# Optimization experiments

Measured on AMD Instinct MI355X. Metric: run time of the kernel, lower is better.

## Reference

```python
import jax, jax.numpy as jnp
import numpy as np

BS = 128          # block size for fp8 block-scaled quantization
FP8_MAX = 448.0   # max normal value of float8_e4m3fn


def _weight_quant(w):
    """Quantize weight [O, I] with per-(128x128)-block scales, DeepSeek-V3 style.
    Returns (w_q stored as fp32 holding fp8-representable values, scale [O/BS, I/BS])."""
    O, I = w.shape
    wb = w.reshape(O // BS, BS, I // BS, BS)
    amax = jnp.max(jnp.abs(wb), axis=(1, 3))
    scale = jnp.where(amax == 0, 1.0, amax / FP8_MAX)
    q = (wb / scale[:, None, :, None]).astype(jnp.float8_e4m3fn).astype(jnp.float32)
    return q.reshape(O, I), scale


def _act_qdq(x):
    """act_quant + dequant: per-128-block (last dim) fp8 quantization of activations."""
    T, D = x.shape
    xb = x.reshape(T, D // BS, BS)
    amax = jnp.max(jnp.abs(xb), axis=-1, keepdims=True)
    scale = jnp.where(amax == 0, 1.0, amax / FP8_MAX)
    q = (xb / scale).astype(jnp.float8_e4m3fn).astype(jnp.float32)
    return (q * scale).reshape(T, D)


def _dequant_w(wq, ws):
    O, I = wq.shape
    return (wq.reshape(O // BS, BS, I // BS, BS) * ws[:, None, :, None]).reshape(O, I)


def _linear_fp8(x, wq, ws):
    # fp8_gemm with per-block scales == dequantized GEMM in fp32 accumulate
    return _act_qdq(x) @ _dequant_w(wq, ws).T


def setup_inputs() -> dict:
    T, DIM, INTER = 2048, 4096, 11008
    key = jax.random.key(0)
    kx, k1, k2, k3 = jax.random.split(key, 4)
    x = jax.random.normal(kx, (T, DIM), dtype=jnp.float32)
    w1 = jax.random.normal(k1, (INTER, DIM), dtype=jnp.float32) * 0.02
    w2 = jax.random.normal(k2, (DIM, INTER), dtype=jnp.float32) * 0.02
    w3 = jax.random.normal(k3, (INTER, DIM), dtype=jnp.float32) * 0.02
    w1_q, w1_s = _weight_quant(w1)
    w2_q, w2_s = _weight_quant(w2)
    w3_q, w3_s = _weight_quant(w3)
    return {"x": x, "w1_q": w1_q, "w1_s": w1_s, "w2_q": w2_q, "w2_s": w2_s,
            "w3_q": w3_q, "w3_s": w3_s}


def reference(x, w1_q, w1_s, w2_q, w2_s, w3_q, w3_s):
    # SwiGLU: w2( silu(w1(x)) * w3(x) ), each linear is fp8 block-scaled GEMM
    h = jax.nn.silu(_linear_fp8(x, w1_q, w1_s)) * _linear_fp8(x, w3_q, w3_s)
    return _linear_fp8(h, w2_q, w2_s)
```

## Files before the change

kernel.cpp:

```cpp
#include <hip/hip_runtime.h>
#include <hip/hip_fp8.h>

#define T_DIM 2048
#define D_DIM 4096
#define I_DIM 11008

typedef int v8i __attribute__((ext_vector_type(8)));
typedef float v4f __attribute__((ext_vector_type(4)));

__device__ inline unsigned char to_fp8(float f) {
  return (unsigned char)__hip_cvt_float_to_fp8(f, __HIP_SATFINITE, __HIP_E4M3);
}

__device__ inline void async_copy16(const void* g, void* l) {
  __builtin_amdgcn_global_load_lds((const __attribute__((address_space(1))) void*)g,
                                   (__attribute__((address_space(3))) void*)l, 16, 0, 0);
}

__global__ void quant_x_kernel(const float* __restrict__ X, unsigned char* __restrict__ Q,
                               float* __restrict__ St, const int T, const int D) {
  const int wave = (blockIdx.x << 2) + (threadIdx.x >> 6);
  const int lane = threadIdx.x & 63;
  const int nb = D >> 7;
  const int t = wave / nb;
  const int kb = wave - t * nb;
  const size_t base = (size_t)t * D + ((size_t)kb << 7);
  const float2 v = ((const float2*)(X + base))[lane];
  float a = fmaxf(fabsf(v.x), fabsf(v.y));
#pragma unroll
  for (int off = 32; off > 0; off >>= 1) a = fmaxf(a, __shfl_xor(a, off));
  const float scale = (a == 0.f) ? 1.f : (a / 448.f);
  unsigned short pk = (unsigned short)to_fp8(v.x / scale) |
                      ((unsigned short)to_fp8(v.y / scale) << 8);
  ((unsigned short*)(Q + base))[lane] = pk;
  if (lane == 0) St[(size_t)kb * T + t] = scale;
}

__global__ void silu_mul_quant_kernel(const float* __restrict__ H1, const float* __restrict__ H3,
                                      unsigned char* __restrict__ Q, float* __restrict__ St,
                                      const int T, const int D) {
  const int wave = (blockIdx.x << 2) + (threadIdx.x >> 6);
  const int lane = threadIdx.x & 63;
  const int nb = D >> 7;
  const int t = wave / nb;
  const int kb = wave - t * nb;
  const size_t base = (size_t)t * D + ((size_t)kb << 7);
  const float2 v1 = ((const float2*)(H1 + base))[lane];
  const float2 v3 = ((const float2*)(H3 + base))[lane];
  const float hx = (v1.x / (1.f + expf(-v1.x))) * v3.x;
  const float hy = (v1.y / (1.f + expf(-v1.y))) * v3.y;
  float a = fmaxf(fabsf(hx), fabsf(hy));
#pragma unroll
  for (int off = 32; off > 0; off >>= 1) a = fmaxf(a, __shfl_xor(a, off));
  const float scale = (a == 0.f) ? 1.f : (a / 448.f);
  unsigned short pk = (unsigned short)to_fp8(hx / scale) |
                      ((unsigned short)to_fp8(hy / scale) << 8);
  ((unsigned short*)(Q + base))[lane] = pk;
  if (lane == 0) St[(size_t)kb * T + t] = scale;
}

__global__ void convert_fp8_kernel(const float4* __restrict__ W, unsigned int* __restrict__ Q,
                                   const int n4) {
  const int i = blockIdx.x * 256 + threadIdx.x;
  if (i >= n4) return;
  const float4 f = W[i];
  Q[i] = (unsigned int)to_fp8(f.x) | ((unsigned int)to_fp8(f.y) << 8) |
         ((unsigned int)to_fp8(f.z) << 16) | ((unsigned int)to_fp8(f.w) << 24);
}

__global__ __launch_bounds__(256, 2) void gemm_fp8_bs(
    const unsigned char* __restrict__ A, const float* __restrict__ sAt,
    const unsigned char* __restrict__ B, const float* __restrict__ sB,
    float* __restrict__ C, const int M, const int N, const int K) {
  __shared__ unsigned char As[128 * 128];
  __shared__ unsigned char Bs[128 * 128];

  const int tid = threadIdx.x;
  const int lane = tid & 63;
  const int w = tid >> 6;
  const int wm = (w >> 1) << 6;
  const int wn = (w & 1) << 6;
  const int row16 = lane & 15;
  const int quad = lane >> 4;
  const int m0 = blockIdx.x << 7;
  const int n0 = blockIdx.y << 7;
  const int nkb = K >> 7;

  const int srow = (w << 5) + (lane >> 3);
  const int scol = (lane & 7) << 4;
  const unsigned char* gA = A + (size_t)(m0 + srow) * K + scol;
  const unsigned char* gB = B + (size_t)(n0 + srow) * K + scol;
  unsigned char* lA = &As[w << 12];
  unsigned char* lB = &Bs[w << 12];

  v4f zero = {0.f, 0.f, 0.f, 0.f};
  v4f acc[4][4];
#pragma unroll
  for (int i = 0; i < 4; ++i)
#pragma unroll
    for (int j = 0; j < 4; ++j) acc[i][j] = zero;

  const float* sArow = sAt + m0 + wm + (quad << 2);
  const float* sBrow = sB + (size_t)(n0 >> 7) * nkb;

  for (int kb = 0; kb < nkb; ++kb) {
    __syncthreads();
    const size_t koff = (size_t)kb << 7;
#pragma unroll
    for (int t = 0; t < 4; ++t)
      async_copy16(gA + (size_t)(t * 8) * K + koff, lA + (t << 10));
#pragma unroll
    for (int t = 0; t < 4; ++t)
      async_copy16(gB + (size_t)(t * 8) * K + koff, lB + (t << 10));

    const float sb = sBrow[kb];
    float4 sa[4];
    const float4* sap = (const float4*)(sArow + (size_t)kb * M);
#pragma unroll
    for (int i = 0; i < 4; ++i) sa[i] = sap[i * 4];

    __syncthreads();

    v8i a[4], b[4];
#pragma unroll
    for (int i = 0; i < 4; ++i)
      a[i] = *(const v8i*)&As[((wm + (i << 4) + row16) << 7) + (quad << 5)];
#pragma unroll
    for (int j = 0; j < 4; ++j)
      b[j] = *(const v8i*)&Bs[((wn + (j << 4) + row16) << 7) + (quad << 5)];

#pragma unroll
    for (int i = 0; i < 4; ++i) {
      v4f cs;
      cs.x = sa[i].x * sb; cs.y = sa[i].y * sb;
      cs.z = sa[i].z * sb; cs.w = sa[i].w * sb;
#pragma unroll
      for (int j = 0; j < 4; ++j) {
        v4f p = __builtin_amdgcn_mfma_scale_f32_16x16x128_f8f6f4(
            a[i], b[j], zero, 0, 0, 0, 0x7f7f7f7f, 0, 0x7f7f7f7f);
        acc[i][j] += cs * p;
      }
    }
  }

#pragma unroll
  for (int i = 0; i < 4; ++i) {
    const size_t rbase = (size_t)(m0 + wm + (i << 4) + (quad << 2));
#pragma unroll
    for (int r = 0; r < 4; ++r) {
      float* crow = C + (rbase + r) * N + n0 + wn + row16;
#pragma unroll
      for (int j = 0; j < 4; ++j) crow[j << 4] = acc[i][j][r];
    }
  }
}

extern "C" void kernel_launch(void* const* d_in, const int* in_sizes, int n_in,
                              void* d_out, int out_size, void* d_ws, size_t ws_size,
                              hipStream_t stream) {
  const float* x   = (const float*)d_in[0];
  const float* w1q = (const float*)d_in[1];
  const float* w1s = (const float*)d_in[2];
  const float* w2q = (const float*)d_in[3];
  const float* w2s = (const float*)d_in[4];
  const float* w3q = (const float*)d_in[5];
  const float* w3s = (const float*)d_in[6];

  unsigned char* ws = (unsigned char*)d_ws;
  const size_t SZ_QX = (size_t)T_DIM * D_DIM;
  const size_t SZ_W  = (size_t)I_DIM * D_DIM;
  const size_t SZ_QH = (size_t)T_DIM * I_DIM;
  const size_t SZ_SX = (size_t)(D_DIM / 128) * T_DIM * 4;
  const size_t SZ_SH = (size_t)(I_DIM / 128) * T_DIM * 4;
  const size_t SZ_H  = (size_t)T_DIM * I_DIM * 4;

  unsigned char* qx   = ws;             ws += SZ_QX;
  unsigned char* w1q8 = ws;             ws += SZ_W;
  unsigned char* w3q8 = ws;             ws += SZ_W;
  unsigned char* w2q8 = ws;             ws += SZ_W;
  unsigned char* qh   = ws;             ws += SZ_QH;
  float* sxt = (float*)ws;              ws += SZ_SX;
  float* sht = (float*)ws;              ws += SZ_SH;
  float* h1  = (float*)ws;              ws += SZ_H;
  float* h3  = (float*)ws;              ws += SZ_H;

  quant_x_kernel<<<(T_DIM * (D_DIM / 128)) / 4, 256, 0, stream>>>(x, qx, sxt, T_DIM, D_DIM);

  const int n4w = (int)(SZ_W / 4);
  convert_fp8_kernel<<<(n4w + 255) / 256, 256, 0, stream>>>((const float4*)w1q, (unsigned int*)w1q8, n4w);
  convert_fp8_kernel<<<(n4w + 255) / 256, 256, 0, stream>>>((const float4*)w3q, (unsigned int*)w3q8, n4w);
  convert_fp8_kernel<<<(n4w + 255) / 256, 256, 0, stream>>>((const float4*)w2q, (unsigned int*)w2q8, n4w);

  dim3 g13(T_DIM / 128, I_DIM / 128);
  gemm_fp8_bs<<<g13, 256, 0, stream>>>(qx, sxt, w1q8, w1s, h1, T_DIM, I_DIM, D_DIM);
  gemm_fp8_bs<<<g13, 256, 0, stream>>>(qx, sxt, w3q8, w3s, h3, T_DIM, I_DIM, D_DIM);

  silu_mul_quant_kernel<<<(T_DIM * (I_DIM / 128)) / 4, 256, 0, stream>>>(h1, h3, qh, sht, T_DIM, I_DIM);

  dim3 g2(T_DIM / 128, D_DIM / 128);
  gemm_fp8_bs<<<g2, 256, 0, stream>>>(qh, sht, w2q8, w2s, (float*)d_out, T_DIM, D_DIM, I_DIM);

  (void)in_sizes; (void)n_in; (void)out_size; (void)ws_size;
}
```

Measured before the change: 1.023 ms.

## Double-buffer LDS tiles and XOR-swizzle fp8 GEMM shared memory layout

Splits the fp8 GEMM's shared-memory tiles into two ping-pong buffers. The async global-to-LDS copy of the next K block is issued before the MFMAs on the current block, which also removes one barrier per iteration. The column chunks in LDS are XOR-swizzled by row, and the fragment loads are split into two 16-byte reads at the swizzled offsets, to cut LDS bank conflicts. LDS use per block doubles to 64 KB, which may limit occupancy, and the loop now assumes an even number of K blocks.

```diff
diff --git a/kernel.cpp b/kernel.cpp
--- a/kernel.cpp
+++ b/kernel.cpp
@@ -6,6 +6,7 @@
 #define I_DIM 11008
 
 typedef int v8i __attribute__((ext_vector_type(8)));
+typedef int v4i __attribute__((ext_vector_type(4)));
 typedef float v4f __attribute__((ext_vector_type(4)));
 
 __device__ inline unsigned char to_fp8(float f) {
@@ -72,8 +73,10 @@
     const unsigned char* __restrict__ A, const float* __restrict__ sAt,
     const unsigned char* __restrict__ B, const float* __restrict__ sB,
     float* __restrict__ C, const int M, const int N, const int K) {
-  __shared__ unsigned char As[128 * 128];
-  __shared__ unsigned char Bs[128 * 128];
+  __shared__ __align__(16) unsigned char As0[128 * 128];
+  __shared__ __align__(16) unsigned char Bs0[128 * 128];
+  __shared__ __align__(16) unsigned char As1[128 * 128];
+  __shared__ __align__(16) unsigned char Bs1[128 * 128];
 
   const int tid = threadIdx.x;
   const int lane = tid & 63;
@@ -86,12 +89,18 @@
   const int n0 = blockIdx.y << 7;
   const int nkb = K >> 7;
 
+  const int x7 = row16 & 7;
+  const int off0 = (((quad << 1) ^ x7) << 4);
+  const int off1 = off0 ^ 16;
+
   const int srow = (w << 5) + (lane >> 3);
-  const int scol = (lane & 7) << 4;
+  const int scol = (((lane & 7) ^ (lane >> 3)) << 4);
   const unsigned char* gA = A + (size_t)(m0 + srow) * K + scol;
   const unsigned char* gB = B + (size_t)(n0 + srow) * K + scol;
-  unsigned char* lA = &As[w << 12];
-  unsigned char* lB = &Bs[w << 12];
+  unsigned char* lA0 = &As0[w << 12];
+  unsigned char* lB0 = &Bs0[w << 12];
+  unsigned char* lA1 = &As1[w << 12];
+  unsigned char* lB1 = &Bs1[w << 12];
 
   v4f zero = {0.f, 0.f, 0.f, 0.f};
   v4f acc[4][4];
@@ -103,45 +112,59 @@
   const float* sArow = sAt + m0 + wm + (quad << 2);
   const float* sBrow = sB + (size_t)(n0 >> 7) * nkb;
 
-  for (int kb = 0; kb < nkb; ++kb) {
+#define STAGE_TILE(LA, LB, KB)                                                  \
+  {                                                                             \
+    const size_t koff = (size_t)(KB) << 7;                                      \
+    _Pragma("unroll") for (int t = 0; t < 4; ++t)                               \
+        async_copy16(gA + (size_t)(t * 8) * K + koff, LA + (t << 10));          \
+    _Pragma("unroll") for (int t = 0; t < 4; ++t)                               \
+        async_copy16(gB + (size_t)(t * 8) * K + koff, LB + (t << 10));          \
+  }
+
+#define COMPUTE_TILE(AS, BS, KB)                                                \
+  {                                                                             \
+    const float sb = sBrow[KB];                                                 \
+    const float4* sap = (const float4*)(sArow + (size_t)(KB) * M);              \
+    float4 sa[4];                                                               \
+    _Pragma("unroll") for (int i = 0; i < 4; ++i) sa[i] = sap[i * 4];           \
+    v8i a[4], b[4];                                                             \
+    _Pragma("unroll") for (int i = 0; i < 4; ++i) {                             \
+      const unsigned char* p = (AS) + ((wm + (i << 4) + row16) << 7);           \
+      const v4i lo = *(const v4i*)(p + off0);                                   \
+      const v4i hi = *(const v4i*)(p + off1);                                   \
+      a[i] = __builtin_shufflevector(lo, hi, 0, 1, 2, 3, 4, 5, 6, 7);           \
+    }                                                                           \
+    _Pragma("unroll") for (int j = 0; j < 4; ++j) {                             \
+      const unsigned char* p = (BS) + ((wn + (j << 4) + row16) << 7);           \
+      const v4i lo = *(const v4i*)(p + off0);                                   \
+      const v4i hi = *(const v4i*)(p + off1);                                   \
+      b[j] = __builtin_shufflevector(lo, hi, 0, 1, 2, 3, 4, 5, 6, 7);           \
+    }                                                                           \
+    _Pragma("unroll") for (int i = 0; i < 4; ++i) {                             \
+      v4f cs;                                                                   \
+      cs.x = sa[i].x * sb; cs.y = sa[i].y * sb;                                 \
+      cs.z = sa[i].z * sb; cs.w = sa[i].w * sb;                                 \
+      _Pragma("unroll") for (int j = 0; j < 4; ++j) {                           \
+        v4f pr = __builtin_amdgcn_mfma_scale_f32_16x16x128_f8f6f4(              \
+            a[i], b[j], zero, 0, 0, 0, 0x7f7f7f7f, 0, 0x7f7f7f7f);              \
+        acc[i][j] += cs * pr;                                                   \
+      }                                                                         \
+    }                                                                           \
+  }
+
+  STAGE_TILE(lA0, lB0, 0);
+  __syncthreads();
+
+  for (int kb = 0; kb < nkb; kb += 2) {
+    STAGE_TILE(lA1, lB1, kb + 1);
+    COMPUTE_TILE(As0, Bs0, kb);
     __syncthreads();
-    const size_t koff = (size_t)kb << 7;
-#pragma unroll
-    for (int t = 0; t < 4; ++t)
-      async_copy16(gA + (size_t)(t * 8) * K + koff, lA + (t << 10));
-#pragma unroll
-    for (int t = 0; t < 4; ++t)
-      async_copy16(gB + (size_t)(t * 8) * K + koff, lB + (t << 10));
-
-    const float sb = sBrow[kb];
-    float4 sa[4];
-    const float4* sap = (const float4*)(sArow + (size_t)kb * M);
-#pragma unroll
-    for (int i = 0; i < 4; ++i) sa[i] = sap[i * 4];
-
+    if (kb + 2 < nkb) STAGE_TILE(lA0, lB0, kb + 2);
+    COMPUTE_TILE(As1, Bs1, kb + 1);
     __syncthreads();
-
-    v8i a[4], b[4];
-#pragma unroll
-    for (int i = 0; i < 4; ++i)
-      a[i] = *(const v8i*)&As[((wm + (i << 4) + row16) << 7) + (quad << 5)];
-#pragma unroll
-    for (int j = 0; j < 4; ++j)
-      b[j] = *(const v8i*)&Bs[((wn + (j << 4) + row16) << 7) + (quad << 5)];
-
-#pragma unroll
-    for (int i = 0; i < 4; ++i) {
-      v4f cs;
-      cs.x = sa[i].x * sb; cs.y = sa[i].y * sb;
-      cs.z = sa[i].z * sb; cs.w = sa[i].w * sb;
-#pragma unroll
-      for (int j = 0; j < 4; ++j) {
-        v4f p = __builtin_amdgcn_mfma_scale_f32_16x16x128_f8f6f4(
-            a[i], b[j], zero, 0, 0, 0, 0x7f7f7f7f, 0, 0x7f7f7f7f);
-        acc[i][j] += cs * p;
-      }
-    }
-  }
+  }
+#undef STAGE_TILE
+#undef COMPUTE_TILE
 
 #pragma unroll
   for (int i = 0; i < 4; ++i) {
```

New measurement: 1.065 ms. 1.04x slower.

## Use 256x256 double-buffered fp8 GEMM tiles and fuse w1/w3 launches

Applied to the files above, without the earlier changes.

Replaces the 128x128 single-buffered block-scaled fp8 GEMM with a 512-thread kernel that computes 256x256 output tiles. The next K-block is prefetched into a second LDS buffer with async global-to-LDS copies while the current one is consumed. Tile rows are XOR-swizzled to avoid LDS bank conflicts, and the activation scales are staged in LDS. The MFMA phases are split with barriers and s_setprio. The w1 and w3 GEMMs share one launch by selecting the weight, scale and output pointers from blockIdx.y. The cost is about 128KB of LDS per block, which allows one block per CU, plus heavy register use from 32 accumulators.

```diff
diff --git a/kernel.cpp b/kernel.cpp
--- a/kernel.cpp
+++ b/kernel.cpp
@@ -6,6 +6,7 @@
 #define I_DIM 11008
 
 typedef int v8i __attribute__((ext_vector_type(8)));
+typedef int v4i __attribute__((ext_vector_type(4)));
 typedef float v4f __attribute__((ext_vector_type(4)));
 
 __device__ inline unsigned char to_fp8(float f) {
@@ -68,89 +69,185 @@
          ((unsigned int)to_fp8(f.z) << 16) | ((unsigned int)to_fp8(f.w) << 24);
 }
 
-__global__ __launch_bounds__(256, 2) void gemm_fp8_bs(
+__global__ __launch_bounds__(512, 2) void gemm256_fp8_bs(
     const unsigned char* __restrict__ A, const float* __restrict__ sAt,
-    const unsigned char* __restrict__ B, const float* __restrict__ sB,
-    float* __restrict__ C, const int M, const int N, const int K) {
-  __shared__ unsigned char As[128 * 128];
-  __shared__ unsigned char Bs[128 * 128];
+    const unsigned char* __restrict__ Ba, const float* __restrict__ sBa, float* __restrict__ Ca,
+    const unsigned char* __restrict__ Bb, const float* __restrict__ sBb, float* __restrict__ Cb,
+    const int NY, const int M, const int N, const int K) {
+  __shared__ __align__(16) unsigned char As[2][256 * 128];
+  __shared__ __align__(16) unsigned char Bs[2][256 * 128];
+  __shared__ __align__(16) float sAs[2][256];
+  __shared__ float sbl[192];
 
   const int tid = threadIdx.x;
   const int lane = tid & 63;
   const int w = tid >> 6;
-  const int wm = (w >> 1) << 6;
-  const int wn = (w & 1) << 6;
+  const int wm = w >> 2;
+  const int wn = w & 3;
+  const int wmrow = wm << 7;
+  const int wnrow = wn << 6;
   const int row16 = lane & 15;
   const int quad = lane >> 4;
-  const int m0 = blockIdx.x << 7;
-  const int n0 = blockIdx.y << 7;
   const int nkb = K >> 7;
 
-  const int srow = (w << 5) + (lane >> 3);
-  const int scol = (lane & 7) << 4;
-  const unsigned char* gA = A + (size_t)(m0 + srow) * K + scol;
-  const unsigned char* gB = B + (size_t)(n0 + srow) * K + scol;
-  unsigned char* lA = &As[w << 12];
-  unsigned char* lB = &Bs[w << 12];
+  int by = (int)blockIdx.y;
+  const int sel = by >= NY;
+  if (sel) by -= NY;
+  const unsigned char* B = sel ? Bb : Ba;
+  const float* sB = sel ? sBb : sBa;
+  float* C = sel ? Cb : Ca;
+  const int m0 = (int)blockIdx.x << 8;
+  const int n0 = by << 8;
+
+  {
+    const float* p0 = sB + (size_t)(n0 >> 7) * nkb;
+    if (tid < 2 * nkb) sbl[tid] = p0[tid];
+  }
+
+  const int srow = tid >> 3;
+  const int gcol = (((tid & 7) ^ (srow & 7)) << 4);
+  const unsigned char* gA = A + (size_t)(m0 + srow) * K + gcol;
+  const unsigned char* gB = B + (size_t)(n0 + srow) * K + gcol;
+  const float* gSa = sAt + m0 + (w << 5) + ((lane & 7) << 2);
+
+  const int off0 = (((quad << 1) ^ (row16 & 7)) << 4);
+  const int off1 = off0 ^ 16;
 
   v4f zero = {0.f, 0.f, 0.f, 0.f};
-  v4f acc[4][4];
-#pragma unroll
-  for (int i = 0; i < 4; ++i)
+  v4f acc[8][4];
+#pragma unroll
+  for (int i = 0; i < 8; ++i)
 #pragma unroll
     for (int j = 0; j < 4; ++j) acc[i][j] = zero;
 
-  const float* sArow = sAt + m0 + wm + (quad << 2);
-  const float* sBrow = sB + (size_t)(n0 >> 7) * nkb;
+#define STAGE(c, kb_)                                                           \
+  {                                                                             \
+    const size_t koff_ = (size_t)(kb_) << 7;                                    \
+    _Pragma("unroll") for (int t_ = 0; t_ < 4; ++t_)                            \
+        async_copy16(gA + koff_ + ((size_t)(t_ << 6)) * K,                      \
+                     &As[c][(t_ << 13) + (w << 10)]);                           \
+    _Pragma("unroll") for (int t_ = 0; t_ < 4; ++t_)                            \
+        async_copy16(gB + koff_ + ((size_t)(t_ << 6)) * K,                      \
+                     &Bs[c][(t_ << 13) + (w << 10)]);                           \
+    if (lane < 8) async_copy16(gSa + (size_t)(kb_) * M, &sAs[c][w << 5]);       \
+  }
+
+#define LDA(dst, AP, mi)                                                        \
+  {                                                                             \
+    const unsigned char* p_ = (AP) + ((wmrow + ((mi) << 4) + row16) << 7);      \
+    const v4i lo_ = *(const v4i*)(p_ + off0);                                   \
+    const v4i hi_ = *(const v4i*)(p_ + off1);                                   \
+    dst = __builtin_shufflevector(lo_, hi_, 0, 1, 2, 3, 4, 5, 6, 7);            \
+  }
+
+#define LDB(dst, BP, nj)                                                        \
+  {                                                                             \
+    const unsigned char* p_ = (BP) + ((wnrow + ((nj) << 4) + row16) << 7);      \
+    const v4i lo_ = *(const v4i*)(p_ + off0);                                   \
+    const v4i hi_ = *(const v4i*)(p_ + off1);                                   \
+    dst = __builtin_shufflevector(lo_, hi_, 0, 1, 2, 3, 4, 5, 6, 7);            \
+  }
+
+#define LDCS(H)                                                                 \
+  {                                                                             \
+    const float4 s0_ = *(const float4*)(Sc + wmrow + ((H) << 6) + (quad << 2)); \
+    const float4 s1_ = *(const float4*)(Sc + wmrow + ((H) << 6) + 16 + (quad << 2)); \
+    const float4 s2_ = *(const float4*)(Sc + wmrow + ((H) << 6) + 32 + (quad << 2)); \
+    const float4 s3_ = *(const float4*)(Sc + wmrow + ((H) << 6) + 48 + (quad << 2)); \
+    cs0 = (v4f){s0_.x * sb, s0_.y * sb, s0_.z * sb, s0_.w * sb};                \
+    cs1 = (v4f){s1_.x * sb, s1_.y * sb, s1_.z * sb, s1_.w * sb};                \
+    cs2 = (v4f){s2_.x * sb, s2_.y * sb, s2_.z * sb, s2_.w * sb};                \
+    cs3 = (v4f){s3_.x * sb, s3_.y * sb, s3_.z * sb, s3_.w * sb};                \
+  }
+
+#define MFMA1(af, bf)                                                           \
+  __builtin_amdgcn_mfma_scale_f32_16x16x128_f8f6f4((af), (bf), zero, 0, 0, 0,   \
+                                                   0x7f7f7f7f, 0, 0x7f7f7f7f)
+
+#define MFMA8(H, bL, bR, jL, jR)                                                \
+  {                                                                             \
+    v4f p_;                                                                     \
+    p_ = MFMA1(a0, bL); acc[(H)*4 + 0][jL] += cs0 * p_;                         \
+    p_ = MFMA1(a0, bR); acc[(H)*4 + 0][jR] += cs0 * p_;                         \
+    p_ = MFMA1(a1, bL); acc[(H)*4 + 1][jL] += cs1 * p_;                         \
+    p_ = MFMA1(a1, bR); acc[(H)*4 + 1][jR] += cs1 * p_;                         \
+    p_ = MFMA1(a2, bL); acc[(H)*4 + 2][jL] += cs2 * p_;                         \
+    p_ = MFMA1(a2, bR); acc[(H)*4 + 2][jR] += cs2 * p_;                         \
+    p_ = MFMA1(a3, bL); acc[(H)*4 + 3][jL] += cs3 * p_;                         \
+    p_ = MFMA1(a3, bR); acc[(H)*4 + 3][jR] += cs3 * p_;                         \
+  }
+
+#define PHASE_PRE                                                               \
+  __builtin_amdgcn_s_barrier();                                                 \
+  asm volatile("s_waitcnt lgkmcnt(0)" ::: "memory");                            \
+  __builtin_amdgcn_sched_barrier(0);                                            \
+  __builtin_amdgcn_s_setprio(1);
+
+#define PHASE_POST                                                              \
+  __builtin_amdgcn_s_setprio(0);                                                \
+  __builtin_amdgcn_s_barrier();
+
+  __syncthreads();
+
+  STAGE(0, 0);
+
+  const int sbi = (wn >> 1) * nkb;
 
   for (int kb = 0; kb < nkb; ++kb) {
-    __syncthreads();
-    const size_t koff = (size_t)kb << 7;
-#pragma unroll
-    for (int t = 0; t < 4; ++t)
-      async_copy16(gA + (size_t)(t * 8) * K + koff, lA + (t << 10));
-#pragma unroll
-    for (int t = 0; t < 4; ++t)
-      async_copy16(gB + (size_t)(t * 8) * K + koff, lB + (t << 10));
-
-    const float sb = sBrow[kb];
-    float4 sa[4];
-    const float4* sap = (const float4*)(sArow + (size_t)kb * M);
-#pragma unroll
-    for (int i = 0; i < 4; ++i) sa[i] = sap[i * 4];
-
-    __syncthreads();
-
-    v8i a[4], b[4];
-#pragma unroll
-    for (int i = 0; i < 4; ++i)
-      a[i] = *(const v8i*)&As[((wm + (i << 4) + row16) << 7) + (quad << 5)];
-#pragma unroll
-    for (int j = 0; j < 4; ++j)
-      b[j] = *(const v8i*)&Bs[((wn + (j << 4) + row16) << 7) + (quad << 5)];
-
-#pragma unroll
-    for (int i = 0; i < 4; ++i) {
-      v4f cs;
-      cs.x = sa[i].x * sb; cs.y = sa[i].y * sb;
-      cs.z = sa[i].z * sb; cs.w = sa[i].w * sb;
-#pragma unroll
-      for (int j = 0; j < 4; ++j) {
-        v4f p = __builtin_amdgcn_mfma_scale_f32_16x16x128_f8f6f4(
-            a[i], b[j], zero, 0, 0, 0, 0x7f7f7f7f, 0, 0x7f7f7f7f);
-        acc[i][j] += cs * p;
-      }
+    const int cur = kb & 1;
+    if (kb + 1 < nkb) {
+      STAGE(cur ^ 1, kb + 1);
+      asm volatile("s_waitcnt vmcnt(9)" ::: "memory");
+    } else {
+      asm volatile("s_waitcnt vmcnt(0)" ::: "memory");
     }
-  }
-
-#pragma unroll
-  for (int i = 0; i < 4; ++i) {
-    const size_t rbase = (size_t)(m0 + wm + (i << 4) + (quad << 2));
+    __builtin_amdgcn_s_barrier();
+    __builtin_amdgcn_sched_barrier(0);
+
+    const unsigned char* Ac = As[cur];
+    const unsigned char* Bc = Bs[cur];
+    const float* Sc = sAs[cur];
+    const float sb = sbl[sbi + kb];
+    v8i a0, a1, a2, a3, b0, b1, b2, b3;
+    v4f cs0, cs1, cs2, cs3;
+
+    LDA(a0, Ac, 0); LDA(a1, Ac, 1); LDA(a2, Ac, 2); LDA(a3, Ac, 3);
+    LDB(b0, Bc, 0); LDB(b1, Bc, 1);
+    LDCS(0);
+    PHASE_PRE;
+    MFMA8(0, b0, b1, 0, 1);
+    PHASE_POST;
+    LDB(b2, Bc, 2); LDB(b3, Bc, 3);
+    PHASE_PRE;
+    MFMA8(0, b2, b3, 2, 3);
+    PHASE_POST;
+    LDA(a0, Ac, 4); LDA(a1, Ac, 5); LDA(a2, Ac, 6); LDA(a3, Ac, 7);
+    LDCS(1);
+    PHASE_PRE;
+    MFMA8(1, b0, b1, 0, 1);
+    PHASE_POST;
+    PHASE_PRE;
+    MFMA8(1, b2, b3, 2, 3);
+    PHASE_POST;
+  }
+
+#undef STAGE
+#undef LDA
+#undef LDB
+#undef LDCS
+#undef MFMA1
+#undef MFMA8
+#undef PHASE_PRE
+#undef PHASE_POST
+
+#pragma unroll
+  for (int mi = 0; mi < 8; ++mi) {
+    const size_t rb = (size_t)(m0 + wmrow + (mi << 4) + (quad << 2));
 #pragma unroll
     for (int r = 0; r < 4; ++r) {
-      float* crow = C + (rbase + r) * N + n0 + wn + row16;
-#pragma unroll
-      for (int j = 0; j < 4; ++j) crow[j << 4] = acc[i][j][r];
+      float* crow = C + (rb + r) * N + n0 + wnrow + row16;
+#pragma unroll
+      for (int nj = 0; nj < 4; ++nj) crow[nj << 4] = acc[mi][nj][r];
     }
   }
 }
@@ -191,14 +288,19 @@
   convert_fp8_kernel<<<(n4w + 255) / 256, 256, 0, stream>>>((const float4*)w3q, (unsigned int*)w3q8, n4w);
   convert_fp8_kernel<<<(n4w + 255) / 256, 256, 0, stream>>>((const float4*)w2q, (unsigned int*)w2q8, n4w);
 
-  dim3 g13(T_DIM / 128, I_DIM / 128);
-  gemm_fp8_bs<<<g13, 256, 0, stream>>>(qx, sxt, w1q8, w1s, h1, T_DIM, I_DIM, D_DIM);
-  gemm_fp8_bs<<<g13, 256, 0, stream>>>(qx, sxt, w3q8, w3s, h3, T_DIM, I_DIM, D_DIM);
+  dim3 g13(T_DIM / 256, 2 * (I_DIM / 256));
+  gemm256_fp8_bs<<<g13, 512, 0, stream>>>(qx, sxt,
+                                          w1q8, w1s, h1,
+                                          w3q8, w3s, h3,
+                                          I_DIM / 256, T_DIM, I_DIM, D_DIM);
 
   silu_mul_quant_kernel<<<(T_DIM * (I_DIM / 128)) / 4, 256, 0, stream>>>(h1, h3, qh, sht, T_DIM, I_DIM);
 
-  dim3 g2(T_DIM / 128, D_DIM / 128);
-  gemm_fp8_bs<<<g2, 256, 0, stream>>>(qh, sht, w2q8, w2s, (float*)d_out, T_DIM, D_DIM, I_DIM);
+  dim3 g2(T_DIM / 256, D_DIM / 256);
+  gemm256_fp8_bs<<<g2, 512, 0, stream>>>(qh, sht,
+                                         w2q8, w2s, (float*)d_out,
+                                         w2q8, w2s, (float*)d_out,
+                                         D_DIM / 256, T_DIM, D_DIM, I_DIM);
 
   (void)in_sizes; (void)n_in; (void)out_size; (void)ws_size;
 }
```

Result: slower. 1.209 ms (+18.2%).
